# Optimization experiments

Measured on AMD Instinct MI355X. Metric: run time of the kernel, lower is better.

Reference implementation:

```python
import jax, jax.numpy as jnp
import numpy as np

H, Hh, E, V, OUT, B, S, T, PAD = 512, 256, 512, 50000, 512, 64, 128, 128, 0


def setup_inputs() -> dict:
    key = jax.random.key(0)
    ks = iter(jax.random.split(key, 32))

    def p(shape, scale=0.05):
        return jax.random.normal(next(ks), shape, jnp.float32) * scale

    emb_in = p((V, E)).at[PAD].set(0.0)   # padding_idx row is zero
    emb_out = p((V, E)).at[PAD].set(0.0)
    src_tokens = jax.random.randint(next(ks), (B, S), 1, V)  # avoid pad_idx=0
    dst = jax.random.randint(next(ks), (B, T), 1, V)
    return {
        'src_tokens': src_tokens,
        'src_lengths': jnp.full((B,), S, dtype=jnp.int32),  # full lengths -> pack/pad is identity
        'dst': dst,
        'emb_in': emb_in, 'emb_out': emb_out,
        'enc_w_ih0': p((2, 4 * Hh, E)),   # [dir, 4h, in] layer0
        'enc_w_ih1': p((2, 4 * Hh, H)),   # layer1 input is bidir concat (H)
        'enc_w_hh': p((2, 2, 4 * Hh, Hh)),  # [layer, dir, 4h, h]
        'enc_b_ih': p((2, 2, 4 * Hh)),
        'enc_b_hh': p((2, 2, 4 * Hh)),
        'dec_w_ih0': p((4 * H, H + E)), 'dec_w_hh0': p((4 * H, H)),
        'dec_b_ih0': p((4 * H,)), 'dec_b_hh0': p((4 * H,)),
        'dec_w_ih1': p((4 * H, H)), 'dec_w_hh1': p((4 * H, H)),
        'dec_b_ih1': p((4 * H,)), 'dec_b_hh1': p((4 * H,)),
        'attn_w': p((H, 2 * H)),           # output_proj, bias=False
        'pred_w': p((OUT, H)), 'pred_b': p((OUT,)),
    }


def _lstm_cell(x, h, c, w_ih, w_hh, b_ih, b_hh):
    # torch gate order: i, f, g, o
    g = x @ w_ih.T + h @ w_hh.T + b_ih + b_hh
    i, f, gg, o = jnp.split(g, 4, axis=-1)
    c = jax.nn.sigmoid(f) * c + jax.nn.sigmoid(i) * jnp.tanh(gg)
    h = jax.nn.sigmoid(o) * jnp.tanh(c)
    return h, c


def _run_lstm(xs, w_ih, w_hh, b_ih, b_hh, reverse):
    z = jnp.zeros((xs.shape[1], w_hh.shape[1]), xs.dtype)

    def step(carry, x):
        h, c = _lstm_cell(x, carry[0], carry[1], w_ih, w_hh, b_ih, b_hh)
        return (h, c), h

    (h, c), out = jax.lax.scan(step, (z, z), xs, reverse=reverse)
    return out, h, c


def _forward(src_tokens, dst, emb_in, emb_out, enc_w_ih0, enc_w_ih1, enc_w_hh,
             enc_b_ih, enc_b_hh, dec_w_ih0, dec_w_hh0, dec_b_ih0, dec_b_hh0,
             dec_w_ih1, dec_w_hh1, dec_b_ih1, dec_b_hh1, attn_w, pred_w, pred_b):
    src = src_tokens.T          # [S, B]
    dst_t = dst.T               # [T, B]
    bsz = src.shape[1]

    # ---- Encoder: 2-layer bidirectional LSTM (sequences are full length) ----
    x = emb_in[src]             # [S, B, E]
    w_ihs = (enc_w_ih0, enc_w_ih1)
    fin_h, fin_c = [], []
    for l in range(2):
        outs = []
        for d, rev in ((0, False), (1, True)):
            o, h, c = _run_lstm(x, w_ihs[l][d], enc_w_hh[l, d], enc_b_ih[l, d], enc_b_hh[l, d], rev)
            outs.append(o)
            fin_h.append(h)
            fin_c.append(c)
        x = jnp.concatenate(outs, axis=-1)   # [S, B, H]
    enc_out = x
    # combine_bidir: per-layer concat of fwd/bwd final states -> [B, H]
    h_l0 = jnp.concatenate(fin_h[0:2], axis=-1)
    h_l1 = jnp.concatenate(fin_h[2:4], axis=-1)
    c_l0 = jnp.concatenate(fin_c[0:2], axis=-1)
    c_l1 = jnp.concatenate(fin_c[2:4], axis=-1)

    enc_mask = (src == PAD)     # [S, B]
    dst_emb = emb_out[dst_t]    # [T, B, E]

    # ---- Decoder: 2 stacked LSTMCells + dot-product attention, input feeding ----
    def dec_step(carry, emb_t):
        h0, c0, h1, c1, feed = carry
        inp = jnp.concatenate((emb_t, feed), axis=1)          # [B, E+H]
        h0, c0 = _lstm_cell(inp, h0, c0, dec_w_ih0, dec_w_hh0, dec_b_ih0, dec_b_hh0)
        h1, c1 = _lstm_cell(h0, h1, c1, dec_w_ih1, dec_w_hh1, dec_b_ih1, dec_b_hh1)
        scores = jnp.einsum('sbh,bh->sb', enc_out, h1)        # [S, B]
        scores = jnp.where(enc_mask, -jnp.inf, scores)
        attn = jax.nn.softmax(scores, axis=0)
        ctx = jnp.einsum('sb,sbh->bh', attn, enc_out)         # [B, H]
        out = jnp.tanh(jnp.concatenate((ctx, h1), axis=1) @ attn_w.T)
        return (h0, c0, h1, c1, out), out

    feed0 = jnp.zeros((bsz, H), dst_emb.dtype)
    _, outs = jax.lax.scan(dec_step, (h_l0, c_l0, h_l1, c_l1, feed0), dst_emb)  # [T, B, H]

    # pred_proj then transpose(1, 2) -> [B, OUT, T]
    res = jnp.einsum('tbh,oh->bot', outs, pred_w) + pred_b[None, :, None]
    return res


def reference(src_tokens, src_lengths, dst, emb_in, emb_out, enc_w_ih0, enc_w_ih1,
              enc_w_hh, enc_b_ih, enc_b_hh, dec_w_ih0, dec_w_hh0, dec_b_ih0,
              dec_b_hh0, dec_w_ih1, dec_w_hh1, dec_b_ih1, dec_b_hh1, attn_w,
              pred_w, pred_b):
    # src_lengths are all == S so pack_padded/pad_packed is an identity
    del src_lengths
    return _forward(src_tokens, dst, emb_in, emb_out, enc_w_ih0, enc_w_ih1,
                    enc_w_hh, enc_b_ih, enc_b_hh, dec_w_ih0, dec_w_hh0,
                    dec_b_ih0, dec_b_hh0, dec_w_ih1, dec_w_hh1, dec_b_ih1,
                    dec_b_hh1, attn_w, pred_w, pred_b)
```

## Files before the change

### kernel.cpp

```cpp
#include <hip/hip_runtime.h>
#include <hip/hip_bf16.h>

#define SS 128
#define TT 128
#define NBLK 256
#define FSTRIDE 16

typedef __attribute__((ext_vector_type(8))) short bf16x8;
typedef __attribute__((ext_vector_type(4))) float f32x4;
typedef unsigned short ushort_t;

__device__ __forceinline__ float sigf(float x) { return 1.f / (1.f + __expf(-x)); }

__device__ __forceinline__ ushort_t f2bf(float f) {
  unsigned b = __builtin_bit_cast(unsigned, f);
  return (ushort_t)((b + 0x7FFFu + ((b >> 16) & 1u)) >> 16);
}
__device__ __forceinline__ float bf2f(ushort_t u) {
  return __builtin_bit_cast(float, (unsigned)u << 16);
}

__device__ __forceinline__ void cstoreh(ushort_t* p, ushort_t v) {
  __hip_atomic_store(p, v, __ATOMIC_RELAXED, __HIP_MEMORY_SCOPE_AGENT);
}

__device__ __forceinline__ int xidx(int k, int b) {
  return (((k >> 5) * 256 + b * 4 + ((k >> 3) & 3)) << 3) + (k & 7);
}

__device__ __forceinline__ void gbar(unsigned* flags, unsigned gen) {
  __syncthreads();
  int tid = threadIdx.x;
  unsigned* arr = flags;
  unsigned* go  = flags + NBLK * FSTRIDE;
  if (blockIdx.x == 0) {
    if (tid > 0) {
      int guard = 0;
      while (__hip_atomic_load(&arr[tid * FSTRIDE], __ATOMIC_RELAXED,
                               __HIP_MEMORY_SCOPE_AGENT) < gen &&
             ++guard < (1 << 20))
        __builtin_amdgcn_s_sleep(1);
    }
    __syncthreads();
    __hip_atomic_store(&go[tid * FSTRIDE], gen, __ATOMIC_RELAXED,
                       __HIP_MEMORY_SCOPE_AGENT);
  } else {
    if (tid == 0) {
      asm volatile("s_waitcnt vmcnt(0)" ::: "memory");
      __hip_atomic_store(&arr[blockIdx.x * FSTRIDE], gen, __ATOMIC_RELAXED,
                         __HIP_MEMORY_SCOPE_AGENT);
      int guard = 0;
      while (__hip_atomic_load(&go[blockIdx.x * FSTRIDE], __ATOMIC_RELAXED,
                               __HIP_MEMORY_SCOPE_AGENT) < gen &&
             ++guard < (1 << 20))
        __builtin_amdgcn_s_sleep(1);
    }
    __syncthreads();
  }
  asm volatile("" ::: "memory");
}

__global__ void k_embed_bf(const float* __restrict__ emb, const int* __restrict__ toks,
                           ushort_t* __restrict__ out, int seqlen) {
  int s = blockIdx.x >> 6, b = blockIdx.x & 63;
  int tok = toks[b * seqlen + s];
  float4 v = ((const float4*)(emb + (size_t)tok * 512))[threadIdx.x];
  unsigned lo = (unsigned)f2bf(v.x) | ((unsigned)f2bf(v.y) << 16);
  unsigned hi = (unsigned)f2bf(v.z) | ((unsigned)f2bf(v.w) << 16);
  uint2 pk = {lo, hi};
  *(uint2*)&out[(size_t)blockIdx.x * 512 + threadIdx.x * 4] = pk;
}

__global__ void k_castw(const float* __restrict__ s0, const float* __restrict__ s1,
                        const float* __restrict__ s2, ushort_t* __restrict__ wBF) {
  int row = blockIdx.x, which = blockIdx.y;
  const float* src = (which == 0) ? s0 + (size_t)row * 512
                   : (which == 1) ? s1 + (size_t)row * 512
                                  : s2 + (size_t)row * 1024;
  float4 v = ((const float4*)src)[threadIdx.x];
  unsigned lo = (unsigned)f2bf(v.x) | ((unsigned)f2bf(v.y) << 16);
  unsigned hi = (unsigned)f2bf(v.z) | ((unsigned)f2bf(v.w) << 16);
  uint2 pk = {lo, hi};
  *(uint2*)&wBF[((size_t)which * 2048 + row) * 512 + threadIdx.x * 4] = pk;
}

__global__ __launch_bounds__(256) void gemm_bf(
    const ushort_t* __restrict__ X, const ushort_t* __restrict__ W,
    const float* __restrict__ b1, const float* __restrict__ b2,
    float* __restrict__ GT) {
  __shared__ ushort_t Xs[128 * 72];
  __shared__ ushort_t Ws[128 * 72];
  __shared__ float sbias[128];
  int n0 = blockIdx.x * 128, m0 = blockIdx.y * 128;
  int tid = threadIdx.x;
  int lane = tid & 63;
  int wv = __builtin_amdgcn_readfirstlane(tid >> 6);
  int h_m = (wv >> 1) * 64, h_n = (wv & 1) * 64;
  int l16 = lane & 15, l4 = (lane >> 4) * 4, k8 = (lane >> 4) * 8;
  if (tid < 128) sbias[tid] = b1[n0 + tid] + b2[n0 + tid];
  f32x4 acc[4][4] = {};
  int lrow = tid >> 1, lhf = (tid & 1) * 32;
  for (int k0 = 0; k0 < 512; k0 += 64) {
    __syncthreads();
    const ushort_t* xs = X + (size_t)(m0 + lrow) * 512 + k0 + lhf;
    const ushort_t* wsrc = W + (size_t)(n0 + lrow) * 512 + k0 + lhf;
#pragma unroll
    for (int q = 0; q < 4; ++q) {
      *(bf16x8*)&Xs[lrow * 72 + lhf + q * 8] = *(const bf16x8*)(xs + q * 8);
      *(bf16x8*)&Ws[lrow * 72 + lhf + q * 8] = *(const bf16x8*)(wsrc + q * 8);
    }
    __syncthreads();
#pragma unroll
    for (int kk = 0; kk < 2; ++kk) {
#pragma unroll
      for (int mt = 0; mt < 4; ++mt) {
        bf16x8 af = *(const bf16x8*)&Xs[(h_m + mt * 16 + l16) * 72 + kk * 32 + k8];
#pragma unroll
        for (int nt = 0; nt < 4; ++nt) {
          bf16x8 bf = *(const bf16x8*)&Ws[(h_n + nt * 16 + l16) * 72 + kk * 32 + k8];
          acc[mt][nt] = __builtin_amdgcn_mfma_f32_16x16x32_bf16(af, bf, acc[mt][nt], 0, 0, 0);
        }
      }
    }
  }
  int s = (m0 + h_m) >> 6;
#pragma unroll
  for (int nt = 0; nt < 4; ++nt) {
    int n = n0 + h_n + nt * 16 + l16;
    float bias = sbias[h_n + nt * 16 + l16];
#pragma unroll
    for (int mt = 0; mt < 4; ++mt) {
      f32x4 v = acc[mt][nt];
      v[0] += bias; v[1] += bias; v[2] += bias; v[3] += bias;
      *(f32x4*)&GT[((size_t)s * 2048 + n) * 64 + mt * 16 + l4] = v;
    }
  }
}

__global__ __launch_bounds__(256) void k_gemm2(
    const float* __restrict__ X, const float* __restrict__ W,
    const float* __restrict__ b1, float* __restrict__ C, int K) {
  __shared__ float Xs[16][132];
  __shared__ float Ws[16][132];
  int m0 = blockIdx.y * 128, n0 = blockIdx.x * 128;
  int tx = threadIdx.x & 15, ty = threadIdx.x >> 4;
  float acc[8][8] = {};
  for (int k0 = 0; k0 < K; k0 += 16) {
    __syncthreads();
#pragma unroll
    for (int j = 0; j < 2; ++j) {
      int f4 = threadIdx.x + j * 256;
      int row = f4 >> 2, kc = (f4 & 3) * 4;
      float4 xv = *(const float4*)&X[(size_t)(m0 + row) * 512 + k0 + kc];
      Xs[kc + 0][row] = xv.x; Xs[kc + 1][row] = xv.y;
      Xs[kc + 2][row] = xv.z; Xs[kc + 3][row] = xv.w;
      float4 wv = *(const float4*)&W[(size_t)(n0 + row) * 512 + k0 + kc];
      Ws[kc + 0][row] = wv.x; Ws[kc + 1][row] = wv.y;
      Ws[kc + 2][row] = wv.z; Ws[kc + 3][row] = wv.w;
    }
    __syncthreads();
#pragma unroll
    for (int kk = 0; kk < 16; ++kk) {
      float a[8], w[8];
      *(float4*)&a[0] = *(const float4*)&Xs[kk][ty * 8];
      *(float4*)&a[4] = *(const float4*)&Xs[kk][ty * 8 + 4];
      *(float4*)&w[0] = *(const float4*)&Ws[kk][tx * 8];
      *(float4*)&w[4] = *(const float4*)&Ws[kk][tx * 8 + 4];
#pragma unroll
      for (int i = 0; i < 8; ++i)
#pragma unroll
        for (int j = 0; j < 8; ++j)
          acc[i][j] += a[i] * w[j];
    }
  }
  for (int i = 0; i < 8; ++i) {
    int m = m0 + ty * 8 + i;
#pragma unroll
    for (int j = 0; j < 8; ++j) {
      int n = n0 + tx * 8 + j;
      C[((size_t)(m & 63) * 512 + n) * 128 + (m >> 6)] = acc[i][j] + b1[n];
    }
  }
}

template<int LOUT>
__global__ __launch_bounds__(256, 1) void enc_persist(
    const float* __restrict__ GT,
    const float* __restrict__ whh,
    ushort_t* __restrict__ ringE,
    void* __restrict__ lout,
    ushort_t* __restrict__ hFin,
    float* __restrict__ cFin,
    unsigned* bar) {
  int nb = blockIdx.x;
  int d = nb >> 7, nbL = nb & 127;
  int tid = threadIdx.x;
  int lane = tid & 63;
  int wv = __builtin_amdgcn_readfirstlane(tid >> 6);
  int l16 = lane & 15, kg = lane >> 4;
  __shared__ ushort_t wE[16 * 264];

  for (int idx = tid; idx < 16 * 256; idx += 256) {
    int m = idx >> 8, k = idx & 255;
    float v = 0.f;
    if (m < 8)
      v = whh[(size_t)d * 262144 +
              (size_t)((m & 3) * 256 + nbL + 128 * (m >> 2)) * 256 + k];
    wE[m * 264 + k] = f2bf(v);
  }
  __syncthreads();

  int b = wv * 16 + l16;
  int hu = nbL + 128 * kg;
  float creg = 0.f;
  const ushort_t* wp = wE + l16 * 264 + kg * 8;

  for (int t = 0; t < SS; ++t) {
    int s = d ? (SS - 1 - t) : t;
    const ushort_t* xb = ringE + (size_t)(t * 2 + d) * 16384 +
                         wv * 512 + l16 * 32 + kg * 8;
    bf16x8 bfr[8];
#pragma unroll
    for (int ks = 0; ks < 8; ++ks) bfr[ks] = *(const bf16x8*)(xb + ks * 2048);
    float gi[4];
    if (lane < 32) {
#pragma unroll
      for (int r = 0; r < 4; ++r)
        gi[r] = GT[((size_t)s * 2048 + d * 1024 + r * 256 + hu) * 64 + b];
    }
    f32x4 acc = {0.f, 0.f, 0.f, 0.f};
#pragma unroll
    for (int ks = 0; ks < 8; ++ks) {
      bf16x8 af = *(const bf16x8*)(wp + ks * 32);
      acc = __builtin_amdgcn_mfma_f32_16x16x32_bf16(af, bfr[ks], acc, 0, 0, 0);
    }
    if (lane < 32) {
      float g4[4];
#pragma unroll
      for (int r = 0; r < 4; ++r) g4[r] = acc[r] + gi[r];
      float ig = sigf(g4[0]), fg = sigf(g4[1]), gg = tanhf(g4[2]), og = sigf(g4[3]);
      creg = fg * creg + ig * gg;
      float hn = og * tanhf(creg);
      cstoreh(&ringE[(size_t)((t + 1) * 2 + d) * 16384 + xidx(hu, b)], f2bf(hn));
      if (LOUT == 0)
        ((ushort_t*)lout)[((size_t)s * 64 + b) * 512 + d * 256 + hu] = f2bf(hn);
      else
        ((float*)lout)[(size_t)b * 65536 + (size_t)s * 512 + d * 256 + hu] = hn;
      if (t == SS - 1) {
        hFin[xidx(512 + d * 256 + hu, b)] = f2bf(hn);
        cFin[(d * 256 + hu) * 64 + b] = creg;
      }
    }
    if (t < SS - 1) gbar(bar, (unsigned)(t + 1));
  }
}

__global__ __launch_bounds__(256, 1) void dec_persist(
    const float* __restrict__ GdT,
    const float* __restrict__ w_ih0, const float* __restrict__ w_hh0,
    const float* __restrict__ w_ih1, const float* __restrict__ w_hh1,
    const float* __restrict__ b_ih1, const float* __restrict__ b_hh1,
    const float* __restrict__ attn_w,
    const float* __restrict__ enc_out,
    const int* __restrict__ src_tokens,
    const float* __restrict__ c0T, const float* __restrict__ c1T,
    ushort_t* __restrict__ r0, ushort_t* __restrict__ r1,
    ushort_t* __restrict__ r2,
    float* __restrict__ houts,
    unsigned* bar) {
  int nb = blockIdx.x;
  int tid = threadIdx.x;
  int lane = tid & 63;
  int wv = __builtin_amdgcn_readfirstlane(tid >> 6);
  int l16 = lane & 15, kg = lane >> 4;
  __shared__ ushort_t wAl[16 * 1032];
  __shared__ ushort_t wBl[16 * 1032];
  __shared__ ushort_t wDl[16 * 1032];
  __shared__ float h1s[512];
  __shared__ float sc[128];

  for (int idx = tid; idx < 16384; idx += 256) {
    int m = idx >> 10, k = idx & 1023;
    float va = 0.f, vb = 0.f, vd = 0.f;
    if (m < 8) {
      int row = (m & 3) * 512 + nb + 256 * (m >> 2);
      va = (k < 512) ? w_ih0[(size_t)row * 1024 + 512 + k]
                     : w_hh0[(size_t)row * 512 + (k - 512)];
      vb = (k < 512) ? w_ih1[(size_t)row * 512 + k]
                     : w_hh1[(size_t)row * 512 + (k - 512)];
    }
    if (m < 2) vd = attn_w[(size_t)(nb * 2 + m) * 1024 + k];
    wAl[m * 1032 + k] = f2bf(va);
    wBl[m * 1032 + k] = f2bf(vb);
    wDl[m * 1032 + k] = f2bf(vd);
  }
  __syncthreads();

  int b = wv * 16 + l16;
  int hu = nb + 256 * kg;
  float c0r = 0.f, c1r = 0.f, bias1[4] = {0.f, 0.f, 0.f, 0.f};
  if (lane < 32) {
    c0r = c0T[hu * 64 + b];
    c1r = c1T[hu * 64 + b];
#pragma unroll
    for (int r = 0; r < 4; ++r)
      bias1[r] = b_ih1[r * 512 + hu] + b_hh1[r * 512 + hu];
  }
  const ushort_t* wpA = wAl + l16 * 1032 + kg * 8;
  const ushort_t* wpB = wBl + l16 * 1032 + kg * 8;
  const ushort_t* wpD = wDl + l16 * 1032 + kg * 8;
  int fragoff = wv * 512 + l16 * 32 + kg * 8;

  for (int t = 0; t < TT; ++t) {
    unsigned gb = (unsigned)(t * 4);
    size_t sC = (size_t)t * 65536, sN = (size_t)(t + 1) * 65536;
    {
      const ushort_t* xb = r0 + sC + fragoff;
      bf16x8 bfr[32];
#pragma unroll
      for (int ks = 0; ks < 32; ++ks) bfr[ks] = *(const bf16x8*)(xb + ks * 2048);
      float giA[4];
      if (lane < 32) {
#pragma unroll
        for (int r = 0; r < 4; ++r)
          giA[r] = GdT[((size_t)t * 2048 + r * 512 + hu) * 64 + b];
      }
      f32x4 acc = {0.f, 0.f, 0.f, 0.f};
#pragma unroll
      for (int ks = 0; ks < 32; ++ks) {
        bf16x8 af = *(const bf16x8*)(wpA + ks * 32);
        acc = __builtin_amdgcn_mfma_f32_16x16x32_bf16(af, bfr[ks], acc, 0, 0, 0);
      }
      if (lane < 32) {
        float g4[4];
#pragma unroll
        for (int r = 0; r < 4; ++r) g4[r] = acc[r] + giA[r];
        float ig = sigf(g4[0]), fg = sigf(g4[1]), gg = tanhf(g4[2]), og = sigf(g4[3]);
        c0r = fg * c0r + ig * gg;
        float hn = og * tanhf(c0r);
        ushort_t hb = f2bf(hn);
        cstoreh(&r0[sN + xidx(512 + hu, b)], hb);
        cstoreh(&r1[sC + xidx(hu, b)], hb);
      }
    }
    gbar(bar, gb + 1);
    {
      const ushort_t* xb = r1 + sC + fragoff;
      bf16x8 bfr[32];
#pragma unroll
      for (int ks = 0; ks < 32; ++ks) bfr[ks] = *(const bf16x8*)(xb + ks * 2048);
      f32x4 acc = {0.f, 0.f, 0.f, 0.f};
#pragma unroll
      for (int ks = 0; ks < 32; ++ks) {
        bf16x8 af = *(const bf16x8*)(wpB + ks * 32);
        acc = __builtin_amdgcn_mfma_f32_16x16x32_bf16(af, bfr[ks], acc, 0, 0, 0);
      }
      if (lane < 32) {
        float g4[4];
#pragma unroll
        for (int r = 0; r < 4; ++r) g4[r] = acc[r] + bias1[r];
        float ig = sigf(g4[0]), fg = sigf(g4[1]), gg = tanhf(g4[2]), og = sigf(g4[3]);
        c1r = fg * c1r + ig * gg;
        float hn = og * tanhf(c1r);
        ushort_t hb = f2bf(hn);
        cstoreh(&r1[sN + xidx(512 + hu, b)], hb);
        cstoreh(&r2[sC + xidx(512 + hu, b)], hb);
      }
    }
    gbar(bar, gb + 2);
    if (nb < 64) {
      const float* eb = enc_out + (size_t)nb * 65536;
      for (int i = tid; i < 512; i += 256)
        h1s[i] = bf2f(r1[sN + xidx(512 + i, nb)]);
      __syncthreads();
      {
        int s2 = tid >> 1, half = tid & 1;
        const float* er = eb + (size_t)s2 * 512 + half * 256;
        const float* hh = h1s + half * 256;
        float a = 0.f;
#pragma unroll 8
        for (int k = 0; k < 256; k += 4) {
          float4 ev = *(const float4*)&er[k];
          a += ev.x * hh[k] + ev.y * hh[k + 1] + ev.z * hh[k + 2] + ev.w * hh[k + 3];
        }
        a += __shfl_xor(a, 1);
        if (!half) sc[s2] = (src_tokens[nb * SS + s2] == 0) ? -1e30f : a;
      }
      __syncthreads();
      if (tid < 64) {
        float m = fmaxf(sc[tid], sc[tid + 64]);
        for (int off = 32; off; off >>= 1) m = fmaxf(m, __shfl_xor(m, off));
        float e0 = __expf(sc[tid] - m), e1 = __expf(sc[tid + 64] - m);
        float ssum = e0 + e1;
        for (int off = 32; off; off >>= 1) ssum += __shfl_xor(ssum, off);
        float inv = 1.f / ssum;
        sc[tid] = e0 * inv; sc[tid + 64] = e1 * inv;
      }
      __syncthreads();
      float a0 = 0.f, a1 = 0.f;
      for (int s2 = 0; s2 < 128; ++s2) {
        float p_ = sc[s2];
        const float* er = eb + (size_t)s2 * 512;
        a0 += p_ * er[tid];
        a1 += p_ * er[tid + 256];
      }
      cstoreh(&r2[sC + xidx(tid, nb)], f2bf(a0));
      cstoreh(&r2[sC + xidx(tid + 256, nb)], f2bf(a1));
    }
    gbar(bar, gb + 3);
    {
      const ushort_t* xb = r2 + sC + fragoff;
      bf16x8 bfr[32];
#pragma unroll
      for (int ks = 0; ks < 32; ++ks) bfr[ks] = *(const bf16x8*)(xb + ks * 2048);
      f32x4 acc = {0.f, 0.f, 0.f, 0.f};
#pragma unroll
      for (int ks = 0; ks < 32; ++ks) {
        bf16x8 af = *(const bf16x8*)(wpD + ks * 32);
        acc = __builtin_amdgcn_mfma_f32_16x16x32_bf16(af, bfr[ks], acc, 0, 0, 0);
      }
      if (lane < 16) {
#pragma unroll
        for (int r = 0; r < 2; ++r) {
          int o = nb * 2 + r;
          float v = tanhf(acc[r]);
          cstoreh(&r0[sN + xidx(o, b)], f2bf(v));
          houts[((size_t)t * 64 + b) * 512 + o] = v;
        }
      }
    }
    if (t < TT - 1) gbar(bar, gb + 4);
  }
}

extern "C" void kernel_launch(void* const* d_in, const int* in_sizes, int n_in,
                              void* d_out, int out_size, void* d_ws, size_t ws_size,
                              hipStream_t stream) {
  const int*   src_tokens = (const int*)d_in[0];
  const int*   dst        = (const int*)d_in[2];
  const float* emb_in     = (const float*)d_in[3];
  const float* emb_out    = (const float*)d_in[4];
  const float* enc_w_ih0  = (const float*)d_in[5];
  const float* enc_w_ih1  = (const float*)d_in[6];
  const float* enc_w_hh   = (const float*)d_in[7];
  const float* enc_b_ih   = (const float*)d_in[8];
  const float* enc_b_hh   = (const float*)d_in[9];
  const float* dec_w_ih0  = (const float*)d_in[10];
  const float* dec_w_hh0  = (const float*)d_in[11];
  const float* dec_b_ih0  = (const float*)d_in[12];
  const float* dec_b_hh0  = (const float*)d_in[13];
  const float* dec_w_ih1  = (const float*)d_in[14];
  const float* dec_w_hh1  = (const float*)d_in[15];
  const float* dec_b_ih1  = (const float*)d_in[16];
  const float* dec_b_hh1  = (const float*)d_in[17];
  const float* attn_w     = (const float*)d_in[18];
  const float* pred_w     = (const float*)d_in[19];
  const float* pred_b     = (const float*)d_in[20];
  float* out = (float*)d_out;

  float* ws      = (float*)d_ws;
  float* houts   = ws;
  float* GT      = ws + 4194304;
  float* encOut  = ws + 20971520;
  ushort_t* r0   = (ushort_t*)(ws + 25165824);
  ushort_t* r1   = (ushort_t*)(ws + 29392896);
  ushort_t* r2   = (ushort_t*)(ws + 33619968);
  ushort_t* wBF  = r2;
  ushort_t* ringE= (ushort_t*)(ws + 37814272);
  float* c0T     = ws + 39927808;
  float* c1T     = ws + 39960576;
  unsigned* barA = (unsigned*)(ws + 39993344);
  unsigned* barB = barA + 8192;
  unsigned* barC = barB + 8192;
  ushort_t* U    = (ushort_t*)(ws + 40017920);

  hipMemsetAsync(barA, 0, 3 * 8192 * sizeof(unsigned), stream);
  hipMemsetAsync(r0, 0, 65536 * sizeof(ushort_t), stream);
  hipMemsetAsync(r1, 0, 65536 * sizeof(ushort_t), stream);
  hipMemsetAsync(ringE, 0, 32768 * sizeof(ushort_t), stream);

  k_castw<<<dim3(2048, 3), 128, 0, stream>>>(enc_w_ih0, enc_w_ih1, dec_w_ih0, wBF);

  k_embed_bf<<<dim3(8192), 128, 0, stream>>>(emb_in, src_tokens, U, SS);
  gemm_bf<<<dim3(16, 64), 256, 0, stream>>>(U, wBF, enc_b_ih, enc_b_hh, GT);
  enc_persist<0><<<dim3(NBLK), 256, 0, stream>>>(GT, enc_w_hh, ringE, U,
                                                 r0, c0T, barA);
  gemm_bf<<<dim3(16, 64), 256, 0, stream>>>(U, wBF + 1048576,
                                            enc_b_ih + 2048, enc_b_hh + 2048, GT);
  enc_persist<1><<<dim3(NBLK), 256, 0, stream>>>(GT, enc_w_hh + 524288, ringE,
                                                 encOut, r1, c1T, barB);

  k_embed_bf<<<dim3(8192), 128, 0, stream>>>(emb_out, dst, U, TT);
  gemm_bf<<<dim3(16, 64), 256, 0, stream>>>(U, wBF + 2097152,
                                            dec_b_ih0, dec_b_hh0, GT);

  dec_persist<<<dim3(NBLK), 256, 0, stream>>>(
      GT, dec_w_ih0, dec_w_hh0, dec_w_ih1, dec_w_hh1, dec_b_ih1, dec_b_hh1,
      attn_w, encOut, src_tokens, c0T, c1T, r0, r1, r2, houts, barC);

  k_gemm2<<<dim3(4, 64), 256, 0, stream>>>(houts, pred_w, pred_b, out, 512);
}
```

Before: 4.858 ms.

## Halve decoder persistent blocks, store encoder output in bf16, use MFMA for projection

The decoder persistent kernel now runs on 128 blocks instead of 256, and each block computes two hidden units per gate with all lanes active. The barrier is templated on block count, so each grid-wide sync involves fewer participants. The layer-1 and attention-projection inputs are read straight from the existing ring buffers instead of duplicated copies. Encoder layer-1 output and decoder outputs are stored as bf16, which halves attention traffic. The final fp32 SIMT projection GEMM is replaced by the bf16 MFMA GEMM with a transposed-store mode, at some cost in precision.

Result: faster. 4.320 ms (-11.1%).

```diff
diff --git a/kernel.cpp b/kernel.cpp
--- a/kernel.cpp
+++ b/kernel.cpp
@@ -4,6 +4,7 @@
 #define SS 128
 #define TT 128
 #define NBLK 256
+#define NBD  128
 #define FSTRIDE 16
 
 typedef __attribute__((ext_vector_type(8))) short bf16x8;
@@ -28,13 +29,14 @@
   return (((k >> 5) * 256 + b * 4 + ((k >> 3) & 3)) << 3) + (k & 7);
 }
 
+template<int NB>
 __device__ __forceinline__ void gbar(unsigned* flags, unsigned gen) {
   __syncthreads();
   int tid = threadIdx.x;
   unsigned* arr = flags;
-  unsigned* go  = flags + NBLK * FSTRIDE;
+  unsigned* go  = flags + NB * FSTRIDE;
   if (blockIdx.x == 0) {
-    if (tid > 0) {
+    if (tid > 0 && tid < NB) {
       int guard = 0;
       while (__hip_atomic_load(&arr[tid * FSTRIDE], __ATOMIC_RELAXED,
                                __HIP_MEMORY_SCOPE_AGENT) < gen &&
@@ -42,8 +44,9 @@
         __builtin_amdgcn_s_sleep(1);
     }
     __syncthreads();
-    __hip_atomic_store(&go[tid * FSTRIDE], gen, __ATOMIC_RELAXED,
-                       __HIP_MEMORY_SCOPE_AGENT);
+    if (tid < NB)
+      __hip_atomic_store(&go[tid * FSTRIDE], gen, __ATOMIC_RELAXED,
+                         __HIP_MEMORY_SCOPE_AGENT);
   } else {
     if (tid == 0) {
       asm volatile("s_waitcnt vmcnt(0)" ::: "memory");
@@ -72,22 +75,28 @@
 }
 
 __global__ void k_castw(const float* __restrict__ s0, const float* __restrict__ s1,
-                        const float* __restrict__ s2, ushort_t* __restrict__ wBF) {
+                        const float* __restrict__ s2, const float* __restrict__ s3,
+                        ushort_t* __restrict__ wBF, ushort_t* __restrict__ predBF) {
   int row = blockIdx.x, which = blockIdx.y;
+  if (which == 3 && row >= 512) return;
   const float* src = (which == 0) ? s0 + (size_t)row * 512
                    : (which == 1) ? s1 + (size_t)row * 512
-                                  : s2 + (size_t)row * 1024;
+                   : (which == 2) ? s2 + (size_t)row * 1024
+                                  : s3 + (size_t)row * 512;
   float4 v = ((const float4*)src)[threadIdx.x];
   unsigned lo = (unsigned)f2bf(v.x) | ((unsigned)f2bf(v.y) << 16);
   unsigned hi = (unsigned)f2bf(v.z) | ((unsigned)f2bf(v.w) << 16);
   uint2 pk = {lo, hi};
-  *(uint2*)&wBF[((size_t)which * 2048 + row) * 512 + threadIdx.x * 4] = pk;
+  if (which == 3)
+    *(uint2*)&predBF[(size_t)row * 512 + threadIdx.x * 4] = pk;
+  else
+    *(uint2*)&wBF[((size_t)which * 2048 + row) * 512 + threadIdx.x * 4] = pk;
 }
 
 __global__ __launch_bounds__(256) void gemm_bf(
     const ushort_t* __restrict__ X, const ushort_t* __restrict__ W,
     const float* __restrict__ b1, const float* __restrict__ b2,
-    float* __restrict__ GT) {
+    float* __restrict__ C, int MODE) {
   __shared__ ushort_t Xs[128 * 72];
   __shared__ ushort_t Ws[128 * 72];
   __shared__ float sbias[128];
@@ -97,7 +106,7 @@
   int wv = __builtin_amdgcn_readfirstlane(tid >> 6);
   int h_m = (wv >> 1) * 64, h_n = (wv & 1) * 64;
   int l16 = lane & 15, l4 = (lane >> 4) * 4, k8 = (lane >> 4) * 8;
-  if (tid < 128) sbias[tid] = b1[n0 + tid] + b2[n0 + tid];
+  if (tid < 128) sbias[tid] = b1[n0 + tid] + (b2 ? b2[n0 + tid] : 0.f);
   f32x4 acc[4][4] = {};
   int lrow = tid >> 1, lhf = (tid & 1) * 32;
   for (int k0 = 0; k0 < 512; k0 += 64) {
@@ -123,62 +132,32 @@
       }
     }
   }
-  int s = (m0 + h_m) >> 6;
-#pragma unroll
-  for (int nt = 0; nt < 4; ++nt) {
-    int n = n0 + h_n + nt * 16 + l16;
-    float bias = sbias[h_n + nt * 16 + l16];
-#pragma unroll
-    for (int mt = 0; mt < 4; ++mt) {
-      f32x4 v = acc[mt][nt];
-      v[0] += bias; v[1] += bias; v[2] += bias; v[3] += bias;
-      *(f32x4*)&GT[((size_t)s * 2048 + n) * 64 + mt * 16 + l4] = v;
-    }
-  }
-}
-
-__global__ __launch_bounds__(256) void k_gemm2(
-    const float* __restrict__ X, const float* __restrict__ W,
-    const float* __restrict__ b1, float* __restrict__ C, int K) {
-  __shared__ float Xs[16][132];
-  __shared__ float Ws[16][132];
-  int m0 = blockIdx.y * 128, n0 = blockIdx.x * 128;
-  int tx = threadIdx.x & 15, ty = threadIdx.x >> 4;
-  float acc[8][8] = {};
-  for (int k0 = 0; k0 < K; k0 += 16) {
-    __syncthreads();
-#pragma unroll
-    for (int j = 0; j < 2; ++j) {
-      int f4 = threadIdx.x + j * 256;
-      int row = f4 >> 2, kc = (f4 & 3) * 4;
-      float4 xv = *(const float4*)&X[(size_t)(m0 + row) * 512 + k0 + kc];
-      Xs[kc + 0][row] = xv.x; Xs[kc + 1][row] = xv.y;
-      Xs[kc + 2][row] = xv.z; Xs[kc + 3][row] = xv.w;
-      float4 wv = *(const float4*)&W[(size_t)(n0 + row) * 512 + k0 + kc];
-      Ws[kc + 0][row] = wv.x; Ws[kc + 1][row] = wv.y;
-      Ws[kc + 2][row] = wv.z; Ws[kc + 3][row] = wv.w;
-    }
-    __syncthreads();
-#pragma unroll
-    for (int kk = 0; kk < 16; ++kk) {
-      float a[8], w[8];
-      *(float4*)&a[0] = *(const float4*)&Xs[kk][ty * 8];
-      *(float4*)&a[4] = *(const float4*)&Xs[kk][ty * 8 + 4];
-      *(float4*)&w[0] = *(const float4*)&Ws[kk][tx * 8];
-      *(float4*)&w[4] = *(const float4*)&Ws[kk][tx * 8 + 4];
-#pragma unroll
-      for (int i = 0; i < 8; ++i)
-#pragma unroll
-        for (int j = 0; j < 8; ++j)
-          acc[i][j] += a[i] * w[j];
-    }
-  }
-  for (int i = 0; i < 8; ++i) {
-    int m = m0 + ty * 8 + i;
-#pragma unroll
-    for (int j = 0; j < 8; ++j) {
-      int n = n0 + tx * 8 + j;
-      C[((size_t)(m & 63) * 512 + n) * 128 + (m >> 6)] = acc[i][j] + b1[n];
+  if (MODE == 1) {
+    int s = (m0 + h_m) >> 6;
+#pragma unroll
+    for (int nt = 0; nt < 4; ++nt) {
+      int n = n0 + h_n + nt * 16 + l16;
+      float bias = sbias[h_n + nt * 16 + l16];
+#pragma unroll
+      for (int mt = 0; mt < 4; ++mt) {
+        f32x4 v = acc[mt][nt];
+        v[0] += bias; v[1] += bias; v[2] += bias; v[3] += bias;
+        *(f32x4*)&C[((size_t)s * 2048 + n) * 64 + mt * 16 + l4] = v;
+      }
+    }
+  } else {
+#pragma unroll
+    for (int nt = 0; nt < 4; ++nt) {
+      int n = n0 + h_n + nt * 16 + l16;
+      float bias = sbias[h_n + nt * 16 + l16];
+#pragma unroll
+      for (int mt = 0; mt < 4; ++mt) {
+#pragma unroll
+        for (int r = 0; r < 4; ++r) {
+          int m = m0 + h_m + mt * 16 + l4 + r;
+          C[((size_t)(m & 63) * 512 + n) * 128 + (m >> 6)] = acc[mt][nt][r] + bias;
+        }
+      }
     }
   }
 }
@@ -188,7 +167,7 @@
     const float* __restrict__ GT,
     const float* __restrict__ whh,
     ushort_t* __restrict__ ringE,
-    void* __restrict__ lout,
+    ushort_t* __restrict__ lout,
     ushort_t* __restrict__ hFin,
     float* __restrict__ cFin,
     unsigned* bar) {
@@ -243,15 +222,15 @@
       float hn = og * tanhf(creg);
       cstoreh(&ringE[(size_t)((t + 1) * 2 + d) * 16384 + xidx(hu, b)], f2bf(hn));
       if (LOUT == 0)
-        ((ushort_t*)lout)[((size_t)s * 64 + b) * 512 + d * 256 + hu] = f2bf(hn);
+        lout[((size_t)s * 64 + b) * 512 + d * 256 + hu] = f2bf(hn);
       else
-        ((float*)lout)[(size_t)b * 65536 + (size_t)s * 512 + d * 256 + hu] = hn;
+        lout[(size_t)b * 65536 + (size_t)s * 512 + d * 256 + hu] = f2bf(hn);
       if (t == SS - 1) {
         hFin[xidx(512 + d * 256 + hu, b)] = f2bf(hn);
         cFin[(d * 256 + hu) * 64 + b] = creg;
       }
     }
-    if (t < SS - 1) gbar(bar, (unsigned)(t + 1));
+    if (t < SS - 1) gbar<NBLK>(bar, (unsigned)(t + 1));
   }
 }
 
@@ -261,12 +240,12 @@
     const float* __restrict__ w_ih1, const float* __restrict__ w_hh1,
     const float* __restrict__ b_ih1, const float* __restrict__ b_hh1,
     const float* __restrict__ attn_w,
-    const float* __restrict__ enc_out,
+    const ushort_t* __restrict__ enc_out,
     const int* __restrict__ src_tokens,
     const float* __restrict__ c0T, const float* __restrict__ c1T,
     ushort_t* __restrict__ r0, ushort_t* __restrict__ r1,
     ushort_t* __restrict__ r2,
-    float* __restrict__ houts,
+    ushort_t* __restrict__ houtsB,
     unsigned* bar) {
   int nb = blockIdx.x;
   int tid = threadIdx.x;
@@ -281,15 +260,13 @@
 
   for (int idx = tid; idx < 16384; idx += 256) {
     int m = idx >> 10, k = idx & 1023;
-    float va = 0.f, vb = 0.f, vd = 0.f;
-    if (m < 8) {
-      int row = (m & 3) * 512 + nb + 256 * (m >> 2);
-      va = (k < 512) ? w_ih0[(size_t)row * 1024 + 512 + k]
-                     : w_hh0[(size_t)row * 512 + (k - 512)];
-      vb = (k < 512) ? w_ih1[(size_t)row * 512 + k]
-                     : w_hh1[(size_t)row * 512 + (k - 512)];
-    }
-    if (m < 2) vd = attn_w[(size_t)(nb * 2 + m) * 1024 + k];
+    int j = m >> 2, g = m & 3;
+    int row = g * 512 + nb + 128 * j;
+    float va = (k < 512) ? w_ih0[(size_t)row * 1024 + 512 + k]
+                         : w_hh0[(size_t)row * 512 + (k - 512)];
+    float vb = (k < 512) ? w_ih1[(size_t)row * 512 + k]
+                         : w_hh1[(size_t)row * 512 + (k - 512)];
+    float vd = (m < 4) ? attn_w[(size_t)(nb * 4 + m) * 1024 + k] : 0.f;
     wAl[m * 1032 + k] = f2bf(va);
     wBl[m * 1032 + k] = f2bf(vb);
     wDl[m * 1032 + k] = f2bf(vd);
@@ -297,15 +274,13 @@
   __syncthreads();
 
   int b = wv * 16 + l16;
-  int hu = nb + 256 * kg;
-  float c0r = 0.f, c1r = 0.f, bias1[4] = {0.f, 0.f, 0.f, 0.f};
-  if (lane < 32) {
-    c0r = c0T[hu * 64 + b];
-    c1r = c1T[hu * 64 + b];
-#pragma unroll
-    for (int r = 0; r < 4; ++r)
-      bias1[r] = b_ih1[r * 512 + hu] + b_hh1[r * 512 + hu];
-  }
+  int hu = nb + 128 * kg;
+  float c0r = c0T[hu * 64 + b];
+  float c1r = c1T[hu * 64 + b];
+  float bias1[4];
+#pragma unroll
+  for (int r = 0; r < 4; ++r)
+    bias1[r] = b_ih1[r * 512 + hu] + b_hh1[r * 512 + hu];
   const ushort_t* wpA = wAl + l16 * 1032 + kg * 8;
   const ushort_t* wpB = wBl + l16 * 1032 + kg * 8;
   const ushort_t* wpD = wDl + l16 * 1032 + kg * 8;
@@ -320,68 +295,63 @@
 #pragma unroll
       for (int ks = 0; ks < 32; ++ks) bfr[ks] = *(const bf16x8*)(xb + ks * 2048);
       float giA[4];
-      if (lane < 32) {
-#pragma unroll
-        for (int r = 0; r < 4; ++r)
-          giA[r] = GdT[((size_t)t * 2048 + r * 512 + hu) * 64 + b];
-      }
+#pragma unroll
+      for (int r = 0; r < 4; ++r)
+        giA[r] = GdT[((size_t)t * 2048 + r * 512 + hu) * 64 + b];
       f32x4 acc = {0.f, 0.f, 0.f, 0.f};
 #pragma unroll
       for (int ks = 0; ks < 32; ++ks) {
         bf16x8 af = *(const bf16x8*)(wpA + ks * 32);
         acc = __builtin_amdgcn_mfma_f32_16x16x32_bf16(af, bfr[ks], acc, 0, 0, 0);
       }
-      if (lane < 32) {
-        float g4[4];
-#pragma unroll
-        for (int r = 0; r < 4; ++r) g4[r] = acc[r] + giA[r];
-        float ig = sigf(g4[0]), fg = sigf(g4[1]), gg = tanhf(g4[2]), og = sigf(g4[3]);
-        c0r = fg * c0r + ig * gg;
-        float hn = og * tanhf(c0r);
-        ushort_t hb = f2bf(hn);
-        cstoreh(&r0[sN + xidx(512 + hu, b)], hb);
-        cstoreh(&r1[sC + xidx(hu, b)], hb);
-      }
-    }
-    gbar(bar, gb + 1);
+      float g4[4];
+#pragma unroll
+      for (int r = 0; r < 4; ++r) g4[r] = acc[r] + giA[r];
+      float ig = sigf(g4[0]), fg = sigf(g4[1]), gg = tanhf(g4[2]), og = sigf(g4[3]);
+      c0r = fg * c0r + ig * gg;
+      float hn = og * tanhf(c0r);
+      cstoreh(&r0[sN + xidx(512 + hu, b)], f2bf(hn));
+    }
+    gbar<NBD>(bar, gb + 1);
     {
-      const ushort_t* xb = r1 + sC + fragoff;
       bf16x8 bfr[32];
-#pragma unroll
-      for (int ks = 0; ks < 32; ++ks) bfr[ks] = *(const bf16x8*)(xb + ks * 2048);
+      const ushort_t* xh0 = r0 + sN + fragoff;
+      const ushort_t* xh1 = r1 + sC + fragoff;
+#pragma unroll
+      for (int ks = 0; ks < 16; ++ks) bfr[ks] = *(const bf16x8*)(xh0 + (16 + ks) * 2048);
+#pragma unroll
+      for (int ks = 16; ks < 32; ++ks) bfr[ks] = *(const bf16x8*)(xh1 + ks * 2048);
       f32x4 acc = {0.f, 0.f, 0.f, 0.f};
 #pragma unroll
       for (int ks = 0; ks < 32; ++ks) {
         bf16x8 af = *(const bf16x8*)(wpB + ks * 32);
         acc = __builtin_amdgcn_mfma_f32_16x16x32_bf16(af, bfr[ks], acc, 0, 0, 0);
       }
-      if (lane < 32) {
-        float g4[4];
-#pragma unroll
-        for (int r = 0; r < 4; ++r) g4[r] = acc[r] + bias1[r];
-        float ig = sigf(g4[0]), fg = sigf(g4[1]), gg = tanhf(g4[2]), og = sigf(g4[3]);
-        c1r = fg * c1r + ig * gg;
-        float hn = og * tanhf(c1r);
-        ushort_t hb = f2bf(hn);
-        cstoreh(&r1[sN + xidx(512 + hu, b)], hb);
-        cstoreh(&r2[sC + xidx(512 + hu, b)], hb);
-      }
-    }
-    gbar(bar, gb + 2);
+      float g4[4];
+#pragma unroll
+      for (int r = 0; r < 4; ++r) g4[r] = acc[r] + bias1[r];
+      float ig = sigf(g4[0]), fg = sigf(g4[1]), gg = tanhf(g4[2]), og = sigf(g4[3]);
+      c1r = fg * c1r + ig * gg;
+      float hn = og * tanhf(c1r);
+      cstoreh(&r1[sN + xidx(512 + hu, b)], f2bf(hn));
+    }
+    gbar<NBD>(bar, gb + 2);
     if (nb < 64) {
-      const float* eb = enc_out + (size_t)nb * 65536;
+      const ushort_t* eb = enc_out + (size_t)nb * 65536;
       for (int i = tid; i < 512; i += 256)
         h1s[i] = bf2f(r1[sN + xidx(512 + i, nb)]);
       __syncthreads();
       {
         int s2 = tid >> 1, half = tid & 1;
-        const float* er = eb + (size_t)s2 * 512 + half * 256;
+        const ushort_t* er = eb + (size_t)s2 * 512 + half * 256;
         const float* hh = h1s + half * 256;
         float a = 0.f;
-#pragma unroll 8
-        for (int k = 0; k < 256; k += 4) {
-          float4 ev = *(const float4*)&er[k];
-          a += ev.x * hh[k] + ev.y * hh[k + 1] + ev.z * hh[k + 2] + ev.w * hh[k + 3];
+#pragma unroll 4
+        for (int k = 0; k < 256; k += 8) {
+          bf16x8 ev = *(const bf16x8*)(er + k);
+#pragma unroll
+          for (int i = 0; i < 8; ++i)
+            a += bf2f((ushort_t)ev[i]) * hh[k + i];
         }
         a += __shfl_xor(a, 1);
         if (!half) sc[s2] = (src_tokens[nb * SS + s2] == 0) ? -1e30f : a;
@@ -400,19 +370,22 @@
       float a0 = 0.f, a1 = 0.f;
       for (int s2 = 0; s2 < 128; ++s2) {
         float p_ = sc[s2];
-        const float* er = eb + (size_t)s2 * 512;
-        a0 += p_ * er[tid];
-        a1 += p_ * er[tid + 256];
+        const ushort_t* er = eb + (size_t)s2 * 512;
+        a0 += p_ * bf2f(er[tid]);
+        a1 += p_ * bf2f(er[tid + 256]);
       }
       cstoreh(&r2[sC + xidx(tid, nb)], f2bf(a0));
       cstoreh(&r2[sC + xidx(tid + 256, nb)], f2bf(a1));
     }
-    gbar(bar, gb + 3);
+    gbar<NBD>(bar, gb + 3);
     {
-      const ushort_t* xb = r2 + sC + fragoff;
       bf16x8 bfr[32];
-#pragma unroll
-      for (int ks = 0; ks < 32; ++ks) bfr[ks] = *(const bf16x8*)(xb + ks * 2048);
+      const ushort_t* xc = r2 + sC + fragoff;
+      const ushort_t* xh1 = r1 + sN + fragoff;
+#pragma unroll
+      for (int ks = 0; ks < 16; ++ks) bfr[ks] = *(const bf16x8*)(xc + ks * 2048);
+#pragma unroll
+      for (int ks = 16; ks < 32; ++ks) bfr[ks] = *(const bf16x8*)(xh1 + ks * 2048);
       f32x4 acc = {0.f, 0.f, 0.f, 0.f};
 #pragma unroll
       for (int ks = 0; ks < 32; ++ks) {
@@ -421,15 +394,16 @@
       }
       if (lane < 16) {
 #pragma unroll
-        for (int r = 0; r < 2; ++r) {
-          int o = nb * 2 + r;
+        for (int r = 0; r < 4; ++r) {
+          int o = nb * 4 + r;
           float v = tanhf(acc[r]);
-          cstoreh(&r0[sN + xidx(o, b)], f2bf(v));
-          houts[((size_t)t * 64 + b) * 512 + o] = v;
+          ushort_t vb = f2bf(v);
+          cstoreh(&r0[sN + xidx(o, b)], vb);
+          houtsB[((size_t)t * 64 + b) * 512 + o] = vb;
         }
       }
     }
-    if (t < TT - 1) gbar(bar, gb + 4);
+    if (t < TT - 1) gbar<NBD>(bar, gb + 4);
   }
 }
 
@@ -458,45 +432,48 @@
   const float* pred_b     = (const float*)d_in[20];
   float* out = (float*)d_out;
 
-  float* ws      = (float*)d_ws;
-  float* houts   = ws;
-  float* GT      = ws + 4194304;
-  float* encOut  = ws + 20971520;
-  ushort_t* r0   = (ushort_t*)(ws + 25165824);
-  ushort_t* r1   = (ushort_t*)(ws + 29392896);
-  ushort_t* r2   = (ushort_t*)(ws + 33619968);
-  ushort_t* wBF  = r2;
-  ushort_t* ringE= (ushort_t*)(ws + 37814272);
-  float* c0T     = ws + 39927808;
-  float* c1T     = ws + 39960576;
-  unsigned* barA = (unsigned*)(ws + 39993344);
-  unsigned* barB = barA + 8192;
-  unsigned* barC = barB + 8192;
-  ushort_t* U    = (ushort_t*)(ws + 40017920);
+  float* ws       = (float*)d_ws;
+  ushort_t* houtsB = (ushort_t*)ws;
+  float* GT       = ws + 4194304;
+  ushort_t* encOutB = (ushort_t*)(ws + 20971520);
+  ushort_t* predBF  = (ushort_t*)(ws + 23068672);
+  ushort_t* r0    = (ushort_t*)(ws + 25165824);
+  ushort_t* r1    = (ushort_t*)(ws + 29392896);
+  ushort_t* r2    = (ushort_t*)(ws + 33619968);
+  ushort_t* wBF   = r2;
+  ushort_t* ringE = (ushort_t*)(ws + 37814272);
+  float* c0T      = ws + 39927808;
+  float* c1T      = ws + 39960576;
+  unsigned* barA  = (unsigned*)(ws + 39993344);
+  unsigned* barB  = barA + 8192;
+  unsigned* barC  = barB + 8192;
+  ushort_t* U     = (ushort_t*)(ws + 40017920);
 
   hipMemsetAsync(barA, 0, 3 * 8192 * sizeof(unsigned), stream);
   hipMemsetAsync(r0, 0, 65536 * sizeof(ushort_t), stream);
   hipMemsetAsync(r1, 0, 65536 * sizeof(ushort_t), stream);
   hipMemsetAsync(ringE, 0, 32768 * sizeof(ushort_t), stream);
 
-  k_castw<<<dim3(2048, 3), 128, 0, stream>>>(enc_w_ih0, enc_w_ih1, dec_w_ih0, wBF);
+  k_castw<<<dim3(2048, 4), 128, 0, stream>>>(enc_w_ih0, enc_w_ih1, dec_w_ih0,
+                                             pred_w, wBF, predBF);
 
   k_embed_bf<<<dim3(8192), 128, 0, stream>>>(emb_in, src_tokens, U, SS);
-  gemm_bf<<<dim3(16, 64), 256, 0, stream>>>(U, wBF, enc_b_ih, enc_b_hh, GT);
+  gemm_bf<<<dim3(16, 64), 256, 0, stream>>>(U, wBF, enc_b_ih, enc_b_hh, GT, 1);
   enc_persist<0><<<dim3(NBLK), 256, 0, stream>>>(GT, enc_w_hh, ringE, U,
                                                  r0, c0T, barA);
   gemm_bf<<<dim3(16, 64), 256, 0, stream>>>(U, wBF + 1048576,
-                                            enc_b_ih + 2048, enc_b_hh + 2048, GT);
+                                            enc_b_ih + 2048, enc_b_hh + 2048, GT, 1);
   enc_persist<1><<<dim3(NBLK), 256, 0, stream>>>(GT, enc_w_hh + 524288, ringE,
-                                                 encOut, r1, c1T, barB);
+                                                 encOutB, r1, c1T, barB);
 
   k_embed_bf<<<dim3(8192), 128, 0, stream>>>(emb_out, dst, U, TT);
   gemm_bf<<<dim3(16, 64), 256, 0, stream>>>(U, wBF + 2097152,
-                                            dec_b_ih0, dec_b_hh0, GT);
-
-  dec_persist<<<dim3(NBLK), 256, 0, stream>>>(
+                                            dec_b_ih0, dec_b_hh0, GT, 1);
+
+  dec_persist<<<dim3(NBD), 256, 0, stream>>>(
       GT, dec_w_ih0, dec_w_hh0, dec_w_ih1, dec_w_hh1, dec_b_ih1, dec_b_hh1,
-      attn_w, encOut, src_tokens, c0T, c1T, r0, r1, r2, houts, barC);
-
-  k_gemm2<<<dim3(4, 64), 256, 0, stream>>>(houts, pred_w, pred_b, out, 512);
-}
+      attn_w, encOutB, src_tokens, c0T, c1T, r0, r1, r2, houtsB, barC);
+
+  gemm_bf<<<dim3(4, 64), 256, 0, stream>>>(houtsB, predBF,
+                                           pred_b, nullptr, out, 2);
+}
```
